# Optimization experiments

Hardware: AMD Instinct MI355X
Metric: run time of the kernel (lower is better)

Reference implementation:

```python
import jax, jax.numpy as jnp
import numpy as np

BETA = 1.0  # lagr_softmax default inverse temperature

def setup_inputs() -> dict:
    key = jax.random.key(0)
    ks = jax.random.split(key, 5)
    B, Tq, Tk, Eq, Ek, E, H = 2, 2048, 2048, 1024, 1024, 1024, 16
    s = lambda d: 1.0 / np.sqrt(d)
    return {
        "gq": jax.random.normal(ks[0], (B, Tq, Eq), jnp.float32),
        "gk": jax.random.normal(ks[1], (B, Tk, Ek), jnp.float32),
        "WQ": jax.random.normal(ks[2], (E, Eq), jnp.float32) * s(Eq),
        "WK": jax.random.normal(ks[3], (E, Ek), jnp.float32) * s(Ek),
        "Wmix": jax.random.normal(ks[4], (1, H), jnp.float32) * s(H),
    }

def reference(gq, gk, WQ, WK, Wmix):
    B, Tq, _ = gq.shape
    H = Wmix.shape[1]
    E = WQ.shape[0]
    D = E // H
    # Linear projections (bias=False): x @ W.T
    q = (gq @ WQ.T).reshape(B, Tq, H, D)          # (B,Tq,H,D)
    k = (gk @ WK.T).reshape(B, -1, H, D)          # (B,Tk,H,D)
    # scores q @ k^T per head: (B,H,Tq,Tk)
    a = jnp.einsum('bqhd,bkhd->bhqk', q, k)
    # mix_heads: Linear(n_heads -> 1) applied over head axis
    a = jnp.einsum('bhqk,h->bqk', a, Wmix[0])     # (B,Tq,Tk)
    # lagr_softmax: (1/beta) * logsumexp(beta * a, dim=-1)
    out = jax.nn.logsumexp(BETA * a, axis=-1) / BETA  # (B,Tq)
    return out[:, None, :]                        # (B,1,Tq) matching torch shape
```

## Files before the change

kernel.cpp:

```cpp
#include <hip/hip_runtime.h>
#include <hip/hip_bf16.h>
#include <math.h>

#define B_    2
#define TQ    2048
#define TK    2048
#define E_    1024
#define MTOT  4096

typedef __attribute__((ext_vector_type(8))) short bf16x8;
typedef __attribute__((ext_vector_type(4))) float f32x4;

__device__ __forceinline__ unsigned short f2bf(float x) {
  unsigned int u = __float_as_uint(x);
  u += 0x7fff + ((u >> 16) & 1);
  return (unsigned short)(u >> 16);
}

__device__ __forceinline__ void load_lds16(const void* g, void* l) {
  __builtin_amdgcn_global_load_lds(
      (const __attribute__((address_space(1))) unsigned int*)g,
      (__attribute__((address_space(3))) unsigned int*)l, 16, 0, 0);
}

#define BARRIER() do { asm volatile("" ::: "memory"); __builtin_amdgcn_s_barrier(); asm volatile("" ::: "memory"); } while (0)
#define WAIT_VM4()   asm volatile("s_waitcnt vmcnt(4)" ::: "memory")
#define WAIT_VM0()   asm volatile("s_waitcnt vmcnt(0)" ::: "memory")
#define WAIT_LGKM0() asm volatile("s_waitcnt lgkmcnt(0)" ::: "memory")


__device__ __forceinline__ void stage_chunk(const unsigned short* gsrc, unsigned short* lds,
                                            int tid, int row0, int kt) {
  const int r  = tid >> 3;
  const int c8 = ((tid & 7) ^ (r & 7)) * 8;
  const unsigned short* g = gsrc + (size_t)(row0 + r) * E_ + (size_t)kt * 64 + c8;
  load_lds16(g, lds + row0 * 64 + tid * 8);
}

#define LDS_AT(base, row, o) ((const bf16x8*)((base) + (((row) * 128 + ((o) ^ (((row) & 7) << 4))) >> 1)))

#define READ_A(mh)                                                            \
  do {                                                                        \
    _Pragma("unroll") for (int f = 0; f < 2; ++f)                             \
      _Pragma("unroll") for (int ks = 0; ks < 2; ++ks)                        \
        a[f][ks] = *LDS_AT(Ac, wm * 64 + (mh) * 32 + f * 16 + li16, ks * 64 + hi4 * 16); \
  } while (0)

#define READ_B(nh)                                                            \
  do {                                                                        \
    _Pragma("unroll") for (int g = 0; g < 2; ++g)                             \
      _Pragma("unroll") for (int ks = 0; ks < 2; ++ks)                        \
        b[nh][g][ks] = *LDS_AT(Bc, wn * 64 + (nh) * 32 + g * 16 + li16, ks * 64 + hi4 * 16); \
  } while (0)

#define MFMA_Q(mh, nh)                                                        \
  do {                                                                        \
    __builtin_amdgcn_s_setprio(1);                                            \
    _Pragma("unroll") for (int ks = 0; ks < 2; ++ks)                          \
      _Pragma("unroll") for (int f = 0; f < 2; ++f)                           \
        _Pragma("unroll") for (int g = 0; g < 2; ++g)                         \
          acc[(mh) * 2 + f][(nh) * 2 + g] = __builtin_amdgcn_mfma_f32_16x16x32_bf16( \
              a[f][ks], b[nh][g][ks], acc[(mh) * 2 + f][(nh) * 2 + g], 0, 0, 0); \
    __builtin_amdgcn_s_setprio(0);                                            \
  } while (0)

#define GEMM_PIPELINE()                                                       \
  do {                                                                        \
    stage_chunk(Ag, As[0], tid, 0, 0);  stage_chunk(Ag, As[0], tid, 64, 0);   \
    stage_chunk(Bg, Bs[0], tid, 0, 0);  stage_chunk(Bg, Bs[0], tid, 64, 0);   \
    stage_chunk(Bg, Bs[0], tid, 128, 0); stage_chunk(Bg, Bs[0], tid, 192, 0); \
    stage_chunk(Bg, Bs[1], tid, 0, 1);  stage_chunk(Bg, Bs[1], tid, 64, 1);   \
    stage_chunk(Bg, Bs[1], tid, 128, 1); stage_chunk(Bg, Bs[1], tid, 192, 1); \
    WAIT_VM4();                                                               \
    BARRIER();                                                                \
    for (int t = 0; t < 16; ++t) {                                            \
      const int c = t & 1;                                                    \
      const int nx = (t + 1) & 15;                                            \
      const int nx2 = (t + 2) & 15;                                           \
      unsigned short* Ac = As[c];                                             \
      unsigned short* Bc = Bs[c];                                             \
                                                                     \
      READ_A(0); READ_B(0);                                                   \
      stage_chunk(Ag, As[c ^ 1], tid, 0, nx);                                 \
      BARRIER(); WAIT_LGKM0(); MFMA_Q(0, 0); BARRIER();                       \
                                                                     \
      READ_B(1);                                                              \
      stage_chunk(Ag, As[c ^ 1], tid, 64, nx);                                \
      BARRIER(); WAIT_LGKM0(); MFMA_Q(0, 1); BARRIER();                       \
                                                                     \
      READ_A(1);                                                              \
      stage_chunk(Bg, Bs[c], tid, 0, nx2);                                    \
      stage_chunk(Bg, Bs[c], tid, 64, nx2);                                   \
      BARRIER(); WAIT_LGKM0(); MFMA_Q(1, 0); BARRIER();                       \
                                                                     \
      stage_chunk(Bg, Bs[c], tid, 128, nx2);                                  \
      stage_chunk(Bg, Bs[c], tid, 192, nx2);                                  \
      WAIT_VM4(); BARRIER(); MFMA_Q(1, 1); BARRIER();                         \
    }                                                                         \
  } while (0)

__global__ void prep_kernel(const float* __restrict__ gq, const float* __restrict__ gk,
                            const float* __restrict__ WQ, const float* __restrict__ WK,
                            const float* __restrict__ Wmix,
                            unsigned short* __restrict__ gqb, unsigned short* __restrict__ gkb,
                            unsigned short* __restrict__ wqb, unsigned short* __restrict__ wkb) {
  const int NGQ = (B_ * TQ * E_) / 4;
  const int NW  = (E_ * E_) / 4;
  const int total = 2 * NGQ + 2 * NW;
  for (int idx = blockIdx.x * blockDim.x + threadIdx.x; idx < total;
       idx += gridDim.x * blockDim.x) {
    const float4* src; unsigned short* dst; int local; float scale = 1.0f;
    if (idx < NGQ)            { src = (const float4*)gq; dst = gqb; local = idx; }
    else if (idx < 2 * NGQ)   { src = (const float4*)gk; dst = gkb; local = idx - NGQ; }
    else if (idx < 2*NGQ+NW)  { src = (const float4*)WQ; dst = wqb; local = idx - 2*NGQ;
                                scale = Wmix[local >> 14]; }
    else                      { src = (const float4*)WK; dst = wkb; local = idx - 2*NGQ - NW; }
    float4 v = src[local];
    ushort4 o;
    o.x = f2bf(v.x * scale); o.y = f2bf(v.y * scale);
    o.z = f2bf(v.z * scale); o.w = f2bf(v.w * scale);
    ((ushort4*)dst)[local] = o;
  }
}

__global__ __launch_bounds__(512, 2) void proj_kernel(
    const unsigned short* __restrict__ gqb, const unsigned short* __restrict__ gkb,
    const unsigned short* __restrict__ wqb, const unsigned short* __restrict__ wkb,
    unsigned short* __restrict__ qp, unsigned short* __restrict__ kp) {
  __shared__ __align__(16) unsigned short As[2][8192];
  __shared__ __align__(16) unsigned short Bs[2][16384];
  const int m0 = blockIdx.y * 128, n0 = blockIdx.x * 256;
  const unsigned short* Ag = (blockIdx.z ? gkb : gqb) + (size_t)m0 * E_;
  const unsigned short* Bg = (blockIdx.z ? wkb : wqb) + (size_t)n0 * E_;
  unsigned short* C        = (blockIdx.z ? kp  : qp);
  const int tid = threadIdx.x, wave = tid >> 6, lane = tid & 63;
  const int wm = wave >> 2, wn = wave & 3, li16 = lane & 15, hi4 = lane >> 4;
  f32x4 acc[4][4] = {};
  bf16x8 a[2][2];
  bf16x8 b[2][2][2];
  GEMM_PIPELINE();
#pragma unroll
  for (int mr = 0; mr < 4; ++mr)
#pragma unroll
    for (int nr = 0; nr < 4; ++nr)
#pragma unroll
      for (int j = 0; j < 4; ++j) {
        int row = m0 + wm * 64 + mr * 16 + hi4 * 4 + j;
        int col = n0 + wn * 64 + nr * 16 + li16;
        C[(size_t)row * E_ + col] = f2bf(acc[mr][nr][j]);
      }
  WAIT_VM0();
}

__global__ __launch_bounds__(512, 2) void score_lse_kernel(
    const unsigned short* __restrict__ qp, const unsigned short* __restrict__ kp,
    float2* __restrict__ partials) {
  __shared__ __align__(16) unsigned short As[2][8192];
  __shared__ __align__(16) unsigned short Bs[2][16384];
  __shared__ float redM[4][128];
  __shared__ float redS[4][128];
  const int bb = blockIdx.z;
  const int m0 = blockIdx.y * 128, n0 = blockIdx.x * 256;
  const unsigned short* Ag = qp + (size_t)bb * TQ * E_ + (size_t)m0 * E_;
  const unsigned short* Bg = kp + (size_t)bb * TK * E_ + (size_t)n0 * E_;
  const int tid = threadIdx.x, wave = tid >> 6, lane = tid & 63;
  const int wm = wave >> 2, wn = wave & 3, li16 = lane & 15, hi4 = lane >> 4;
  f32x4 acc[4][4] = {};
  bf16x8 a[2][2];
  bf16x8 b[2][2][2];
  GEMM_PIPELINE();
#pragma unroll
  for (int mr = 0; mr < 4; ++mr) {
#pragma unroll
    for (int j = 0; j < 4; ++j) {
      float m = fmaxf(fmaxf(acc[mr][0][j], acc[mr][1][j]),
                      fmaxf(acc[mr][2][j], acc[mr][3][j]));
#pragma unroll
      for (int msk = 1; msk < 16; msk <<= 1) m = fmaxf(m, __shfl_xor(m, msk, 64));
      float s = 0.f;
#pragma unroll
      for (int nr = 0; nr < 4; ++nr) s += expf(acc[mr][nr][j] - m);
#pragma unroll
      for (int msk = 1; msk < 16; msk <<= 1) s += __shfl_xor(s, msk, 64);
      if (li16 == 0) {
        int row = wm * 64 + mr * 16 + hi4 * 4 + j;
        redM[wn][row] = m;
        redS[wn][row] = s;
      }
    }
  }
  __syncthreads();
  if (tid < 128) {
    float M = fmaxf(fmaxf(redM[0][tid], redM[1][tid]), fmaxf(redM[2][tid], redM[3][tid]));
    float S = redS[0][tid] * expf(redM[0][tid] - M) + redS[1][tid] * expf(redM[1][tid] - M) +
              redS[2][tid] * expf(redM[2][tid] - M) + redS[3][tid] * expf(redM[3][tid] - M);
    int qrow = bb * TQ + m0 + tid;
    partials[(size_t)qrow * 8 + blockIdx.x] = make_float2(M, S);
  }
}

__global__ void finalize_kernel(const float2* __restrict__ partials, float* __restrict__ out) {
  int r = blockIdx.x * blockDim.x + threadIdx.x;
  if (r >= MTOT) return;
  const float2* p = partials + (size_t)r * 8;
  float M = p[0].x;
#pragma unroll
  for (int i = 1; i < 8; ++i) M = fmaxf(M, p[i].x);
  float S = 0.f;
#pragma unroll
  for (int i = 0; i < 8; ++i) S += p[i].y * expf(p[i].x - M);
  out[r] = logf(S) + M;
}

extern "C" void kernel_launch(void* const* d_in, const int* in_sizes, int n_in,
                              void* d_out, int out_size, void* d_ws, size_t ws_size,
                              hipStream_t stream) {
  const float* gq   = (const float*)d_in[0];
  const float* gk   = (const float*)d_in[1];
  const float* WQ   = (const float*)d_in[2];
  const float* WK   = (const float*)d_in[3];
  const float* Wmix = (const float*)d_in[4];
  float* out = (float*)d_out;

  char* ws = (char*)d_ws;
  unsigned short* gqb = (unsigned short*)(ws);
  unsigned short* gkb = (unsigned short*)(ws + 8388608);
  unsigned short* wqb = (unsigned short*)(ws + 16777216);
  unsigned short* wkb = (unsigned short*)(ws + 18874368);
  unsigned short* qp  = (unsigned short*)(ws + 20971520);
  unsigned short* kp  = (unsigned short*)(ws + 29360128);
  float2* partials    = (float2*)(ws + 37748736);

  hipLaunchKernelGGL(prep_kernel, dim3(1024), dim3(256), 0, stream,
                     gq, gk, WQ, WK, Wmix, gqb, gkb, wqb, wkb);
  hipLaunchKernelGGL(proj_kernel, dim3(4, 32, 2), dim3(512), 0, stream,
                     gqb, gkb, wqb, wkb, qp, kp);
  hipLaunchKernelGGL(score_lse_kernel, dim3(8, 16, 2), dim3(512), 0, stream,
                     qp, kp, partials);
  hipLaunchKernelGGL(finalize_kernel, dim3(16), dim3(256), 0, stream,
                     partials, out);
}
```

Baseline: 148.4 us.

## Switch GEMMs to 128x128 tiles with 4 waves and simpler double-buffered pipeline

```diff
diff --git a/kernel.cpp b/kernel.cpp
--- a/kernel.cpp
+++ b/kernel.cpp
@@ -24,78 +24,62 @@
 }
 
 #define BARRIER() do { asm volatile("" ::: "memory"); __builtin_amdgcn_s_barrier(); asm volatile("" ::: "memory"); } while (0)
-#define WAIT_VM4()   asm volatile("s_waitcnt vmcnt(4)" ::: "memory")
-#define WAIT_VM0()   asm volatile("s_waitcnt vmcnt(0)" ::: "memory")
-#define WAIT_LGKM0() asm volatile("s_waitcnt lgkmcnt(0)" ::: "memory")
-
-
-__device__ __forceinline__ void stage_chunk(const unsigned short* gsrc, unsigned short* lds,
-                                            int tid, int row0, int kt) {
+#define WAIT_VM8()   do { asm volatile("s_waitcnt vmcnt(8)" ::: "memory"); __builtin_amdgcn_sched_barrier(0); } while (0)
+#define WAIT_VM0()   do { asm volatile("s_waitcnt vmcnt(0)" ::: "memory"); __builtin_amdgcn_sched_barrier(0); } while (0)
+#define WAIT_LGKM0() do { asm volatile("s_waitcnt lgkmcnt(0)" ::: "memory"); __builtin_amdgcn_sched_barrier(0); } while (0)
+
+
+__device__ __forceinline__ void stage_tile(const unsigned short* gsrc, unsigned short* lds,
+                                           int tid, int kt) {
   const int r  = tid >> 3;
   const int c8 = ((tid & 7) ^ (r & 7)) * 8;
-  const unsigned short* g = gsrc + (size_t)(row0 + r) * E_ + (size_t)kt * 64 + c8;
-  load_lds16(g, lds + row0 * 64 + tid * 8);
+  const unsigned short* g = gsrc + (size_t)r * E_ + (size_t)kt * 64 + c8;
+  unsigned short* l = lds + tid * 8;
+#pragma unroll
+  for (int i = 0; i < 4; ++i)
+    load_lds16(g + (size_t)(32 * i) * E_, l + 2048 * i);
 }
 
 #define LDS_AT(base, row, o) ((const bf16x8*)((base) + (((row) * 128 + ((o) ^ (((row) & 7) << 4))) >> 1)))
 
-#define READ_A(mh)                                                            \
+#define READ_ALL()                                                            \
   do {                                                                        \
-    _Pragma("unroll") for (int f = 0; f < 2; ++f)                             \
-      _Pragma("unroll") for (int ks = 0; ks < 2; ++ks)                        \
-        a[f][ks] = *LDS_AT(Ac, wm * 64 + (mh) * 32 + f * 16 + li16, ks * 64 + hi4 * 16); \
+    _Pragma("unroll") for (int f = 0; f < 4; ++f)                             \
+      _Pragma("unroll") for (int ks = 0; ks < 2; ++ks) {                      \
+        a[f][ks] = *LDS_AT(Ac, wm * 64 + f * 16 + li16, ks * 64 + hi4 * 16);  \
+        b[f][ks] = *LDS_AT(Bc, wn * 64 + f * 16 + li16, ks * 64 + hi4 * 16);  \
+      }                                                                       \
   } while (0)
 
-#define READ_B(nh)                                                            \
-  do {                                                                        \
-    _Pragma("unroll") for (int g = 0; g < 2; ++g)                             \
-      _Pragma("unroll") for (int ks = 0; ks < 2; ++ks)                        \
-        b[nh][g][ks] = *LDS_AT(Bc, wn * 64 + (nh) * 32 + g * 16 + li16, ks * 64 + hi4 * 16); \
-  } while (0)
-
-#define MFMA_Q(mh, nh)                                                        \
+#define MFMA_ALL()                                                            \
   do {                                                                        \
     __builtin_amdgcn_s_setprio(1);                                            \
     _Pragma("unroll") for (int ks = 0; ks < 2; ++ks)                          \
-      _Pragma("unroll") for (int f = 0; f < 2; ++f)                           \
-        _Pragma("unroll") for (int g = 0; g < 2; ++g)                         \
-          acc[(mh) * 2 + f][(nh) * 2 + g] = __builtin_amdgcn_mfma_f32_16x16x32_bf16( \
-              a[f][ks], b[nh][g][ks], acc[(mh) * 2 + f][(nh) * 2 + g], 0, 0, 0); \
+      _Pragma("unroll") for (int f = 0; f < 4; ++f)                           \
+        _Pragma("unroll") for (int g = 0; g < 4; ++g)                         \
+          acc[f][g] = __builtin_amdgcn_mfma_f32_16x16x32_bf16(                \
+              a[f][ks], b[g][ks], acc[f][g], 0, 0, 0);                        \
     __builtin_amdgcn_s_setprio(0);                                            \
   } while (0)
 
 #define GEMM_PIPELINE()                                                       \
   do {                                                                        \
-    stage_chunk(Ag, As[0], tid, 0, 0);  stage_chunk(Ag, As[0], tid, 64, 0);   \
-    stage_chunk(Bg, Bs[0], tid, 0, 0);  stage_chunk(Bg, Bs[0], tid, 64, 0);   \
-    stage_chunk(Bg, Bs[0], tid, 128, 0); stage_chunk(Bg, Bs[0], tid, 192, 0); \
-    stage_chunk(Bg, Bs[1], tid, 0, 1);  stage_chunk(Bg, Bs[1], tid, 64, 1);   \
-    stage_chunk(Bg, Bs[1], tid, 128, 1); stage_chunk(Bg, Bs[1], tid, 192, 1); \
-    WAIT_VM4();                                                               \
+    stage_tile(Ag, As[0], tid, 0); stage_tile(Bg, Bs[0], tid, 0);             \
+    stage_tile(Ag, As[1], tid, 1); stage_tile(Bg, Bs[1], tid, 1);             \
+    WAIT_VM8();                                                               \
     BARRIER();                                                                \
     for (int t = 0; t < 16; ++t) {                                            \
       const int c = t & 1;                                                    \
-      const int nx = (t + 1) & 15;                                            \
-      const int nx2 = (t + 2) & 15;                                           \
       unsigned short* Ac = As[c];                                             \
       unsigned short* Bc = Bs[c];                                             \
-                                                                     \
-      READ_A(0); READ_B(0);                                                   \
-      stage_chunk(Ag, As[c ^ 1], tid, 0, nx);                                 \
-      BARRIER(); WAIT_LGKM0(); MFMA_Q(0, 0); BARRIER();                       \
-                                                                     \
-      READ_B(1);                                                              \
-      stage_chunk(Ag, As[c ^ 1], tid, 64, nx);                                \
-      BARRIER(); WAIT_LGKM0(); MFMA_Q(0, 1); BARRIER();                       \
-                                                                     \
-      READ_A(1);                                                              \
-      stage_chunk(Bg, Bs[c], tid, 0, nx2);                                    \
-      stage_chunk(Bg, Bs[c], tid, 64, nx2);                                   \
-      BARRIER(); WAIT_LGKM0(); MFMA_Q(1, 0); BARRIER();                       \
-                                                                     \
-      stage_chunk(Bg, Bs[c], tid, 128, nx2);                                  \
-      stage_chunk(Bg, Bs[c], tid, 192, nx2);                                  \
-      WAIT_VM4(); BARRIER(); MFMA_Q(1, 1); BARRIER();                         \
+      READ_ALL();                                                             \
+      WAIT_LGKM0();                     \
+      BARRIER();                            \
+      stage_tile(Ag, As[c], tid, (t + 2) & 15);                               \
+      stage_tile(Bg, Bs[c], tid, (t + 2) & 15);                               \
+      MFMA_ALL();                       \
+      WAIT_VM8();                     \
+      BARRIER();                                                              \
     }                                                                         \
   } while (0)
 
@@ -123,67 +107,67 @@
   }
 }
 
-__global__ __launch_bounds__(512, 2) void proj_kernel(
+__global__ __launch_bounds__(256, 2) void proj_kernel(
     const unsigned short* __restrict__ gqb, const unsigned short* __restrict__ gkb,
     const unsigned short* __restrict__ wqb, const unsigned short* __restrict__ wkb,
     unsigned short* __restrict__ qp, unsigned short* __restrict__ kp) {
   __shared__ __align__(16) unsigned short As[2][8192];
-  __shared__ __align__(16) unsigned short Bs[2][16384];
-  const int m0 = blockIdx.y * 128, n0 = blockIdx.x * 256;
+  __shared__ __align__(16) unsigned short Bs[2][8192];
+  const int m0 = blockIdx.y * 128, n0 = blockIdx.x * 128;
   const unsigned short* Ag = (blockIdx.z ? gkb : gqb) + (size_t)m0 * E_;
   const unsigned short* Bg = (blockIdx.z ? wkb : wqb) + (size_t)n0 * E_;
   unsigned short* C        = (blockIdx.z ? kp  : qp);
   const int tid = threadIdx.x, wave = tid >> 6, lane = tid & 63;
-  const int wm = wave >> 2, wn = wave & 3, li16 = lane & 15, hi4 = lane >> 4;
+  const int wm = wave >> 1, wn = wave & 1, li16 = lane & 15, hi4 = lane >> 4;
   f32x4 acc[4][4] = {};
-  bf16x8 a[2][2];
-  bf16x8 b[2][2][2];
+  bf16x8 a[4][2];
+  bf16x8 b[4][2];
   GEMM_PIPELINE();
 #pragma unroll
-  for (int mr = 0; mr < 4; ++mr)
-#pragma unroll
-    for (int nr = 0; nr < 4; ++nr)
+  for (int f = 0; f < 4; ++f)
+#pragma unroll
+    for (int g = 0; g < 4; ++g)
 #pragma unroll
       for (int j = 0; j < 4; ++j) {
-        int row = m0 + wm * 64 + mr * 16 + hi4 * 4 + j;
-        int col = n0 + wn * 64 + nr * 16 + li16;
-        C[(size_t)row * E_ + col] = f2bf(acc[mr][nr][j]);
+        int row = m0 + wm * 64 + f * 16 + hi4 * 4 + j;
+        int col = n0 + wn * 64 + g * 16 + li16;
+        C[(size_t)row * E_ + col] = f2bf(acc[f][g][j]);
       }
   WAIT_VM0();
 }
 
-__global__ __launch_bounds__(512, 2) void score_lse_kernel(
+__global__ __launch_bounds__(256, 2) void score_lse_kernel(
     const unsigned short* __restrict__ qp, const unsigned short* __restrict__ kp,
     float2* __restrict__ partials) {
   __shared__ __align__(16) unsigned short As[2][8192];
-  __shared__ __align__(16) unsigned short Bs[2][16384];
-  __shared__ float redM[4][128];
-  __shared__ float redS[4][128];
+  __shared__ __align__(16) unsigned short Bs[2][8192];
+  __shared__ float redM[2][128];
+  __shared__ float redS[2][128];
   const int bb = blockIdx.z;
-  const int m0 = blockIdx.y * 128, n0 = blockIdx.x * 256;
+  const int m0 = blockIdx.y * 128, n0 = blockIdx.x * 128;
   const unsigned short* Ag = qp + (size_t)bb * TQ * E_ + (size_t)m0 * E_;
   const unsigned short* Bg = kp + (size_t)bb * TK * E_ + (size_t)n0 * E_;
   const int tid = threadIdx.x, wave = tid >> 6, lane = tid & 63;
-  const int wm = wave >> 2, wn = wave & 3, li16 = lane & 15, hi4 = lane >> 4;
+  const int wm = wave >> 1, wn = wave & 1, li16 = lane & 15, hi4 = lane >> 4;
   f32x4 acc[4][4] = {};
-  bf16x8 a[2][2];
-  bf16x8 b[2][2][2];
+  bf16x8 a[4][2];
+  bf16x8 b[4][2];
   GEMM_PIPELINE();
 #pragma unroll
-  for (int mr = 0; mr < 4; ++mr) {
+  for (int f = 0; f < 4; ++f) {
 #pragma unroll
     for (int j = 0; j < 4; ++j) {
-      float m = fmaxf(fmaxf(acc[mr][0][j], acc[mr][1][j]),
-                      fmaxf(acc[mr][2][j], acc[mr][3][j]));
+      float m = fmaxf(fmaxf(acc[f][0][j], acc[f][1][j]),
+                      fmaxf(acc[f][2][j], acc[f][3][j]));
 #pragma unroll
       for (int msk = 1; msk < 16; msk <<= 1) m = fmaxf(m, __shfl_xor(m, msk, 64));
       float s = 0.f;
 #pragma unroll
-      for (int nr = 0; nr < 4; ++nr) s += expf(acc[mr][nr][j] - m);
+      for (int g = 0; g < 4; ++g) s += expf(acc[f][g][j] - m);
 #pragma unroll
       for (int msk = 1; msk < 16; msk <<= 1) s += __shfl_xor(s, msk, 64);
       if (li16 == 0) {
-        int row = wm * 64 + mr * 16 + hi4 * 4 + j;
+        int row = wm * 64 + f * 16 + hi4 * 4 + j;
         redM[wn][row] = m;
         redS[wn][row] = s;
       }
@@ -191,24 +175,24 @@
   }
   __syncthreads();
   if (tid < 128) {
-    float M = fmaxf(fmaxf(redM[0][tid], redM[1][tid]), fmaxf(redM[2][tid], redM[3][tid]));
-    float S = redS[0][tid] * expf(redM[0][tid] - M) + redS[1][tid] * expf(redM[1][tid] - M) +
-              redS[2][tid] * expf(redM[2][tid] - M) + redS[3][tid] * expf(redM[3][tid] - M);
+    float mA = redM[0][tid], mB = redM[1][tid];
+    float M = fmaxf(mA, mB);
+    float S = redS[0][tid] * expf(mA - M) + redS[1][tid] * expf(mB - M);
     int qrow = bb * TQ + m0 + tid;
-    partials[(size_t)qrow * 8 + blockIdx.x] = make_float2(M, S);
+    partials[(size_t)qrow * 16 + blockIdx.x] = make_float2(M, S);
   }
 }
 
 __global__ void finalize_kernel(const float2* __restrict__ partials, float* __restrict__ out) {
   int r = blockIdx.x * blockDim.x + threadIdx.x;
   if (r >= MTOT) return;
-  const float2* p = partials + (size_t)r * 8;
+  const float2* p = partials + (size_t)r * 16;
   float M = p[0].x;
 #pragma unroll
-  for (int i = 1; i < 8; ++i) M = fmaxf(M, p[i].x);
+  for (int i = 1; i < 16; ++i) M = fmaxf(M, p[i].x);
   float S = 0.f;
 #pragma unroll
-  for (int i = 0; i < 8; ++i) S += p[i].y * expf(p[i].x - M);
+  for (int i = 0; i < 16; ++i) S += p[i].y * expf(p[i].x - M);
   out[r] = logf(S) + M;
 }
 
@@ -233,9 +217,9 @@
 
   hipLaunchKernelGGL(prep_kernel, dim3(1024), dim3(256), 0, stream,
                      gq, gk, WQ, WK, Wmix, gqb, gkb, wqb, wkb);
-  hipLaunchKernelGGL(proj_kernel, dim3(4, 32, 2), dim3(512), 0, stream,
+  hipLaunchKernelGGL(proj_kernel, dim3(8, 32, 2), dim3(256), 0, stream,
                      gqb, gkb, wqb, wkb, qp, kp);
-  hipLaunchKernelGGL(score_lse_kernel, dim3(8, 16, 2), dim3(512), 0, stream,
+  hipLaunchKernelGGL(score_lse_kernel, dim3(16, 16, 2), dim3(256), 0, stream,
                      qp, kp, partials);
   hipLaunchKernelGGL(finalize_kernel, dim3(16), dim3(256), 0, stream,
                      partials, out);
```

Measured after the change: 137.9 us. -7.1%, faster.
